# Kernel tuning notes

Hardware: AMD Instinct MI355X
Metric: run time of the kernel (lower is better)

Reference implementation:

```python
import jax, jax.numpy as jnp
import numpy as np

SEQ_LEN = 2048
EMB_DIM = 1024
HIDDEN = 1024
VOCAB = 50257
OUT = 50257


def setup_inputs() -> dict:
    key = jax.random.key(0)
    ks = jax.random.split(key, 8)
    s = 0.02
    input_seq = jax.random.randint(ks[0], (SEQ_LEN,), 0, VOCAB)
    emb = jax.random.normal(ks[1], (VOCAB, EMB_DIM), dtype=jnp.float32) * s
    # PyTorch nn.LSTM params: weight_ih [4H, E], weight_hh [4H, H], biases [4H]
    W_ih = jax.random.normal(ks[2], (4 * HIDDEN, EMB_DIM), dtype=jnp.float32) * s
    W_hh = jax.random.normal(ks[3], (4 * HIDDEN, HIDDEN), dtype=jnp.float32) * s
    b_ih = jax.random.normal(ks[4], (4 * HIDDEN,), dtype=jnp.float32) * s
    b_hh = jax.random.normal(ks[5], (4 * HIDDEN,), dtype=jnp.float32) * s
    W_out = jax.random.normal(ks[6], (OUT, HIDDEN), dtype=jnp.float32) * s
    b_out = jax.random.normal(ks[7], (OUT,), dtype=jnp.float32) * s
    return {"input_seq": input_seq, "emb": emb, "W_ih": W_ih, "W_hh": W_hh,
            "b_ih": b_ih, "b_hh": b_hh, "W_out": W_out, "b_out": b_out}


def _lstm_forward(x, W_ih, W_hh, b_ih, b_hh):
    # x: [S, E]; batch dim (=1 in the torch module) is collapsed away.
    H = W_hh.shape[1]
    # Precompute input contribution to all gates for every timestep: [S, 4H]
    x_gates = x @ W_ih.T + (b_ih + b_hh)

    def step(carry, xg):
        h, c = carry
        g = xg + h @ W_hh.T  # [4H]
        i, f, gg, o = jnp.split(g, 4)  # PyTorch gate order: i, f, g, o
        i = jax.nn.sigmoid(i)
        f = jax.nn.sigmoid(f)
        gg = jnp.tanh(gg)
        o = jax.nn.sigmoid(o)
        c = f * c + i * gg
        h = o * jnp.tanh(c)
        return (h, c), h

    h0 = jnp.zeros((H,), dtype=x.dtype)
    c0 = jnp.zeros((H,), dtype=x.dtype)
    _, hs = jax.lax.scan(step, (h0, c0), x_gates)
    return hs  # [S, H]


def reference(input_seq, emb, W_ih, W_hh, b_ih, b_hh, W_out, b_out):
    x = emb[input_seq]  # [S, E] embedding lookup
    hs = _lstm_forward(x, W_ih, W_hh, b_ih, b_hh)  # [S, H]
    logits = hs @ W_out.T + b_out  # [S, OUT]
    return jax.nn.log_softmax(logits, axis=1)
```

## Files before the change

### kernel.cpp

```cpp
#include <hip/hip_runtime.h>
#include <hip/hip_bf16.h>

#define SEQ 2048
#define EMB 1024
#define HID 1024
#define G4  4096
#define VOC 50257
#define VPAD 50304
#define KDIM 1024

typedef short bhalf8 __attribute__((ext_vector_type(8)));
typedef float f32x4  __attribute__((ext_vector_type(4)));

typedef __attribute__((address_space(3))) void lds_void;
typedef __attribute__((address_space(1))) const void gbl_cvoid;

__device__ __forceinline__ void direct_lds16(void* lds, const void* g) {
    __builtin_amdgcn_global_load_lds((gbl_cvoid*)g, (lds_void*)lds, 16, 0, 0);
}

__device__ __forceinline__ unsigned short f2b(float f) {
    unsigned u = __float_as_uint(f);
    unsigned r = u + 0x7fffu + ((u >> 16) & 1u);
    return (unsigned short)(r >> 16);
}

__global__ void f32_to_bf16_k(const float* __restrict__ src, unsigned short* __restrict__ dst,
                              long n_src, long n_dst) {
    long i = ((long)blockIdx.x * 256 + threadIdx.x) * 4;
    if (i >= n_dst) return;
    unsigned short o0 = 0, o1 = 0, o2 = 0, o3 = 0;
    if (i < n_src) {
        f32x4 v = *(const f32x4*)&src[i];
        o0 = f2b(v[0]); o1 = f2b(v[1]); o2 = f2b(v[2]); o3 = f2b(v[3]);
    }
    ushort4 o; o.x = o0; o.y = o1; o.z = o2; o.w = o3;
    *(ushort4*)&dst[i] = o;
}

__global__ void embed_cvt_k(const int* __restrict__ seq, const float* __restrict__ emb,
                            unsigned short* __restrict__ xb) {
    int s = blockIdx.x;
    int k = threadIdx.x * 4;
    long row = (long)seq[s] * EMB;
    f32x4 v = *(const f32x4*)&emb[row + k];
    ushort4 o; o.x = f2b(v[0]); o.y = f2b(v[1]); o.z = f2b(v[2]); o.w = f2b(v[3]);
    *(ushort4*)&xb[(long)s * EMB + k] = o;
}

__global__ void bias_sum_k(const float* __restrict__ a, const float* __restrict__ b,
                           float* __restrict__ o) {
    int i = blockIdx.x * 256 + threadIdx.x;
    if (i < G4) o[i] = a[i] + b[i];
}

__global__ __launch_bounds__(256)
void gemm_bt_k(const unsigned short* __restrict__ A, const unsigned short* __restrict__ Bt,
               const float* __restrict__ bias, float* __restrict__ C,
               int M, int Nreal, int K, int ldc) {
    __shared__ unsigned short lA[128 * 64];
    __shared__ unsigned short lB[128 * 64];
    const int tid  = threadIdx.x;
    const int wave = tid >> 6;
    const int lane = tid & 63;
    const int m0 = blockIdx.x * 128;
    const int n0 = blockIdx.y * 128;
    const int wm = (wave >> 1) * 64;
    const int wn = (wave & 1) * 64;
    const int quad = lane >> 4, l16 = lane & 15;
    const int srow = lane >> 3;
    const int scol = (lane & 7) * 8;

    f32x4 acc[4][4] = {};

    for (int k0 = 0; k0 < K; k0 += 64) {
#pragma unroll
        for (int c = 0; c < 4; ++c) {
            int r0 = wave * 32 + c * 8;
            const unsigned short* ga = A  + (long)(m0 + r0 + srow) * K + k0 + scol;
            direct_lds16(&lA[r0 * 64], ga);
            const unsigned short* gb = Bt + (long)(n0 + r0 + srow) * K + k0 + scol;
            direct_lds16(&lB[r0 * 64], gb);
        }
        __syncthreads();
#pragma unroll
        for (int kk = 0; kk < 2; ++kk) {
            bhalf8 af[4], bf[4];
#pragma unroll
            for (int i = 0; i < 4; ++i) {
                af[i] = *(const bhalf8*)&lA[(wm + i * 16 + l16) * 64 + kk * 32 + quad * 8];
                bf[i] = *(const bhalf8*)&lB[(wn + i * 16 + l16) * 64 + kk * 32 + quad * 8];
            }
#pragma unroll
            for (int i = 0; i < 4; ++i)
#pragma unroll
                for (int j = 0; j < 4; ++j)
                    acc[i][j] = __builtin_amdgcn_mfma_f32_16x16x32_bf16(af[i], bf[j], acc[i][j], 0, 0, 0);
        }
        __syncthreads();
    }
#pragma unroll
    for (int i = 0; i < 4; ++i) {
        int gm = m0 + wm + i * 16 + quad * 4;
#pragma unroll
        for (int j = 0; j < 4; ++j) {
            int gn = n0 + wn + j * 16 + l16;
            if (gn < Nreal) {
                float bv = bias[gn];
#pragma unroll
                for (int r = 0; r < 4; ++r)
                    C[(long)(gm + r) * ldc + gn] = acc[i][j][r] + bv;
            }
        }
    }
}

__global__ __launch_bounds__(256, 1)
void lstm_seq_k(const float* __restrict__ W_hh, const float* __restrict__ xg,
                unsigned short* __restrict__ hs_b, unsigned long long* __restrict__ hbuf) {
    const int tid = threadIdx.x;
    const int wg  = blockIdx.x;
    const int lr  = tid >> 4;
    const int seg = tid & 15;
    const int gate = lr >> 2;
    const int ul   = lr & 3;
    const int u    = wg * 4 + ul;
    const int grow = gate * HID + u;

    __shared__ float h_lds[HID];
    __shared__ float g_lds[4][4];

    f32x4 w[16];
#pragma unroll
    for (int m = 0; m < 16; ++m)
        w[m] = *(const f32x4*)&W_hh[(long)grow * HID + (m * 16 + seg) * 4];

#pragma unroll
    for (int q = 0; q < 4; ++q) h_lds[tid + q * 256] = 0.f;
    float c = 0.f;
    __syncthreads();

    for (int t = 0; t < SEQ; ++t) {
        float xgv = (seg == 0) ? xg[(long)t * G4 + grow] : 0.f;
        if (t > 0) {
            const unsigned long long want = (unsigned long long)t;
            unsigned long long* src = &hbuf[((t - 1) & 1) * HID];
#pragma unroll
            for (int q = 0; q < 4; ++q) {
                int e = tid + q * 256;
                unsigned long long v;
                do {
                    v = __hip_atomic_load(&src[e], __ATOMIC_RELAXED, __HIP_MEMORY_SCOPE_AGENT);
                } while ((v >> 32) != want);
                h_lds[e] = __uint_as_float((unsigned)v);
            }
        }
        __syncthreads();

        float acc = 0.f;
        const f32x4* h4 = (const f32x4*)h_lds;
#pragma unroll
        for (int m = 0; m < 16; ++m) {
            f32x4 hv = h4[m * 16 + seg];
            acc += w[m][0] * hv[0] + w[m][1] * hv[1] + w[m][2] * hv[2] + w[m][3] * hv[3];
        }
        acc += __shfl_xor(acc, 8);
        acc += __shfl_xor(acc, 4);
        acc += __shfl_xor(acc, 2);
        acc += __shfl_xor(acc, 1);

        if (seg == 0) {
            float g = acc + xgv;
            float a = (gate == 2) ? tanhf(g) : 1.f / (1.f + __expf(-g));
            g_lds[gate][ul] = a;
        }
        __syncthreads();
        if (tid < 4) {
            float iv = g_lds[0][tid], fv = g_lds[1][tid], gv = g_lds[2][tid], ov = g_lds[3][tid];
            c = fv * c + iv * gv;
            float h = ov * tanhf(c);
            int ug = wg * 4 + tid;
            hs_b[(long)t * HID + ug] = f2b(h);
            unsigned long long pk = ((unsigned long long)(t + 1) << 32) | (unsigned long long)__float_as_uint(h);
            __hip_atomic_store(&hbuf[(t & 1) * HID + ug], pk, __ATOMIC_RELAXED, __HIP_MEMORY_SCOPE_AGENT);
        }
        __syncthreads();
    }
}

__global__ __launch_bounds__(256)
void log_softmax_k(float* __restrict__ X) {
    const int tid = threadIdx.x;
    const long base = (long)blockIdx.x * VOC;
    float* p = X + base;
    const int head = (4 - (int)(base & 3)) & 3;
    const int n4 = (VOC - head) >> 2;
    const int tail_start = head + n4 * 4;
    f32x4* p4 = (f32x4*)(p + head);

    float m = -INFINITY, s = 0.f;
    auto upd = [&](float x) {
        float nm = fmaxf(m, x);
        s = s * __expf(m - nm) + __expf(x - nm);
        m = nm;
    };
    for (int i = tid; i < n4; i += 256) {
        f32x4 v = p4[i];
        upd(v[0]); upd(v[1]); upd(v[2]); upd(v[3]);
    }
    if (tid == 0) {
        for (int i = 0; i < head; ++i) upd(p[i]);
        for (int i = tail_start; i < VOC; ++i) upd(p[i]);
    }
#pragma unroll
    for (int o = 32; o; o >>= 1) {
        float m2 = __shfl_xor(m, o), s2 = __shfl_xor(s, o);
        float nm = fmaxf(m, m2);
        s = s * __expf(m - nm) + s2 * __expf(m2 - nm);
        m = nm;
    }
    __shared__ float sm[4], ss[4], sL;
    if ((tid & 63) == 0) { sm[tid >> 6] = m; ss[tid >> 6] = s; }
    __syncthreads();
    if (tid == 0) {
        m = sm[0]; s = ss[0];
        for (int wv = 1; wv < 4; ++wv) {
            float m2 = sm[wv], s2 = ss[wv];
            float nm = fmaxf(m, m2);
            s = s * __expf(m - nm) + s2 * __expf(m2 - nm);
            m = nm;
        }
        sL = m + __logf(s);
    }
    __syncthreads();
    const float L = sL;
    for (int i = tid; i < n4; i += 256) {
        f32x4 v = p4[i];
        v[0] -= L; v[1] -= L; v[2] -= L; v[3] -= L;
        p4[i] = v;
    }
    if (tid == 0) {
        for (int i = 0; i < head; ++i) p[i] -= L;
        for (int i = tail_start; i < VOC; ++i) p[i] -= L;
    }
}

extern "C" void kernel_launch(void* const* d_in, const int* in_sizes, int n_in,
                              void* d_out, int out_size, void* d_ws, size_t ws_size,
                              hipStream_t stream) {
    const int*   seq   = (const int*)d_in[0];
    const float* emb   = (const float*)d_in[1];
    const float* W_ih  = (const float*)d_in[2];
    const float* W_hh  = (const float*)d_in[3];
    const float* b_ih  = (const float*)d_in[4];
    const float* b_hh  = (const float*)d_in[5];
    const float* W_out = (const float*)d_in[6];
    const float* b_out = (const float*)d_in[7];
    float* out = (float*)d_out;

    size_t off = 0;
    auto carve = [&](size_t bytes) {
        void* p = (char*)d_ws + off;
        off += (bytes + 255) & ~(size_t)255;
        return p;
    };
    unsigned short* wWout = (unsigned short*)carve((size_t)VPAD * KDIM * 2);
    unsigned short* wWih  = (unsigned short*)carve((size_t)G4 * KDIM * 2);
    unsigned short* wX    = (unsigned short*)carve((size_t)SEQ * EMB * 2);
    unsigned short* wHs   = (unsigned short*)carve((size_t)SEQ * HID * 2);
    float*          wXg   = (float*)carve((size_t)SEQ * G4 * 4);
    float*          wBsum = (float*)carve((size_t)G4 * 4);
    unsigned long long* wHbuf = (unsigned long long*)carve((size_t)2 * HID * 8);

    f32_to_bf16_k<<<(int)(((size_t)VPAD * KDIM / 4 + 255) / 256), 256, 0, stream>>>(
        W_out, wWout, (long)VOC * KDIM, (long)VPAD * KDIM);
    f32_to_bf16_k<<<(int)(((size_t)G4 * KDIM / 4 + 255) / 256), 256, 0, stream>>>(
        W_ih, wWih, (long)G4 * KDIM, (long)G4 * KDIM);
    embed_cvt_k<<<SEQ, 256, 0, stream>>>(seq, emb, wX);
    bias_sum_k<<<(G4 + 255) / 256, 256, 0, stream>>>(b_ih, b_hh, wBsum);

    gemm_bt_k<<<dim3(SEQ / 128, G4 / 128), 256, 0, stream>>>(
        wX, wWih, wBsum, wXg, SEQ, G4, KDIM, G4);

    lstm_seq_k<<<256, 256, 0, stream>>>(W_hh, wXg, wHs, wHbuf);

    gemm_bt_k<<<dim3(SEQ / 128, VPAD / 128), 256, 0, stream>>>(
        wHs, wWout, b_out, out, SEQ, VOC, KDIM, VOC);

    log_softmax_k<<<SEQ, 256, 0, stream>>>(out);
}
```

Before: 6.388 ms.

## Restructure LSTM step so each wave owns one unit, cutting barriers per step

```diff
diff --git a/kernel.cpp b/kernel.cpp
--- a/kernel.cpp
+++ b/kernel.cpp
@@ -23,6 +23,13 @@
     unsigned u = __float_as_uint(f);
     unsigned r = u + 0x7fffu + ((u >> 16) & 1u);
     return (unsigned short)(r >> 16);
+}
+
+__device__ __forceinline__ float fast_sig(float x) {
+    return __frcp_rn(1.f + __expf(-x));
+}
+__device__ __forceinline__ float fast_tanh(float x) {
+    return 1.f - 2.f * __frcp_rn(__expf(2.f * x) + 1.f);
 }
 
 __global__ void f32_to_bf16_k(const float* __restrict__ src, unsigned short* __restrict__ dst,
@@ -118,73 +125,92 @@
 __global__ __launch_bounds__(256, 1)
 void lstm_seq_k(const float* __restrict__ W_hh, const float* __restrict__ xg,
                 unsigned short* __restrict__ hs_b, unsigned long long* __restrict__ hbuf) {
-    const int tid = threadIdx.x;
-    const int wg  = blockIdx.x;
-    const int lr  = tid >> 4;
-    const int seg = tid & 15;
-    const int gate = lr >> 2;
-    const int ul   = lr & 3;
-    const int u    = wg * 4 + ul;
-    const int grow = gate * HID + u;
-
-    __shared__ float h_lds[HID];
-    __shared__ float g_lds[4][4];
-
-    f32x4 w[16];
-#pragma unroll
-    for (int m = 0; m < 16; ++m)
-        w[m] = *(const f32x4*)&W_hh[(long)grow * HID + (m * 16 + seg) * 4];
-
-#pragma unroll
-    for (int q = 0; q < 4; ++q) h_lds[tid + q * 256] = 0.f;
+    const int tid  = threadIdx.x;
+    const int wg   = blockIdx.x;
+    const int wave = tid >> 6;
+    const int lane = tid & 63;
+    const int u    = wg * 4 + wave;
+
+    __shared__ float h_lds[2][HID];
+
+    f32x4 w[4][4];
+#pragma unroll
+    for (int g = 0; g < 4; ++g)
+#pragma unroll
+        for (int m = 0; m < 4; ++m)
+            w[g][m] = *(const f32x4*)&W_hh[(long)(g * HID + u) * HID + (m * 64 + lane) * 4];
+
+#pragma unroll
+    for (int q = 0; q < 4; ++q) h_lds[0][tid + q * 256] = 0.f;
     float c = 0.f;
+
+    float xc0 = xg[0 * HID + u];
+    float xc1 = xg[1 * HID + u];
+    float xc2 = xg[2 * HID + u];
+    float xc3 = xg[3 * HID + u];
     __syncthreads();
 
     for (int t = 0; t < SEQ; ++t) {
-        float xgv = (seg == 0) ? xg[(long)t * G4 + grow] : 0.f;
+        const int pb = t & 1;
         if (t > 0) {
             const unsigned long long want = (unsigned long long)t;
-            unsigned long long* src = &hbuf[((t - 1) & 1) * HID];
-#pragma unroll
-            for (int q = 0; q < 4; ++q) {
-                int e = tid + q * 256;
-                unsigned long long v;
-                do {
-                    v = __hip_atomic_load(&src[e], __ATOMIC_RELAXED, __HIP_MEMORY_SCOPE_AGENT);
-                } while ((v >> 32) != want);
-                h_lds[e] = __uint_as_float((unsigned)v);
+            unsigned long long* src = &hbuf[(pb ^ 1) * HID];
+            unsigned long long v0, v1, v2, v3;
+            for (;;) {
+                v0 = __hip_atomic_load(&src[tid],       __ATOMIC_RELAXED, __HIP_MEMORY_SCOPE_AGENT);
+                v1 = __hip_atomic_load(&src[tid + 256], __ATOMIC_RELAXED, __HIP_MEMORY_SCOPE_AGENT);
+                v2 = __hip_atomic_load(&src[tid + 512], __ATOMIC_RELAXED, __HIP_MEMORY_SCOPE_AGENT);
+                v3 = __hip_atomic_load(&src[tid + 768], __ATOMIC_RELAXED, __HIP_MEMORY_SCOPE_AGENT);
+                if (((v0 >> 32) == want) & ((v1 >> 32) == want) &
+                    ((v2 >> 32) == want) & ((v3 >> 32) == want)) break;
             }
+            float* hb = h_lds[pb];
+            hb[tid]       = __uint_as_float((unsigned)v0);
+            hb[tid + 256] = __uint_as_float((unsigned)v1);
+            hb[tid + 512] = __uint_as_float((unsigned)v2);
+            hb[tid + 768] = __uint_as_float((unsigned)v3);
         }
         __syncthreads();
 
-        float acc = 0.f;
-        const f32x4* h4 = (const f32x4*)h_lds;
-#pragma unroll
-        for (int m = 0; m < 16; ++m) {
-            f32x4 hv = h4[m * 16 + seg];
-            acc += w[m][0] * hv[0] + w[m][1] * hv[1] + w[m][2] * hv[2] + w[m][3] * hv[3];
-        }
-        acc += __shfl_xor(acc, 8);
-        acc += __shfl_xor(acc, 4);
-        acc += __shfl_xor(acc, 2);
-        acc += __shfl_xor(acc, 1);
-
-        if (seg == 0) {
-            float g = acc + xgv;
-            float a = (gate == 2) ? tanhf(g) : 1.f / (1.f + __expf(-g));
-            g_lds[gate][ul] = a;
-        }
-        __syncthreads();
-        if (tid < 4) {
-            float iv = g_lds[0][tid], fv = g_lds[1][tid], gv = g_lds[2][tid], ov = g_lds[3][tid];
-            c = fv * c + iv * gv;
-            float h = ov * tanhf(c);
-            int ug = wg * 4 + tid;
-            hs_b[(long)t * HID + ug] = f2b(h);
-            unsigned long long pk = ((unsigned long long)(t + 1) << 32) | (unsigned long long)__float_as_uint(h);
-            __hip_atomic_store(&hbuf[(t & 1) * HID + ug], pk, __ATOMIC_RELAXED, __HIP_MEMORY_SCOPE_AGENT);
-        }
-        __syncthreads();
+        float xn0 = 0.f, xn1 = 0.f, xn2 = 0.f, xn3 = 0.f;
+        if (t + 1 < SEQ) {
+            const float* xr = xg + (long)(t + 1) * G4;
+            xn0 = xr[0 * HID + u]; xn1 = xr[1 * HID + u];
+            xn2 = xr[2 * HID + u]; xn3 = xr[3 * HID + u];
+        }
+
+        const f32x4* h4 = (const f32x4*)h_lds[pb];
+        float acc0 = 0.f, acc1 = 0.f, acc2 = 0.f, acc3 = 0.f;
+#pragma unroll
+        for (int m = 0; m < 4; ++m) {
+            f32x4 hv = h4[m * 64 + lane];
+            acc0 += w[0][m][0] * hv[0] + w[0][m][1] * hv[1] + w[0][m][2] * hv[2] + w[0][m][3] * hv[3];
+            acc1 += w[1][m][0] * hv[0] + w[1][m][1] * hv[1] + w[1][m][2] * hv[2] + w[1][m][3] * hv[3];
+            acc2 += w[2][m][0] * hv[0] + w[2][m][1] * hv[1] + w[2][m][2] * hv[2] + w[2][m][3] * hv[3];
+            acc3 += w[3][m][0] * hv[0] + w[3][m][1] * hv[1] + w[3][m][2] * hv[2] + w[3][m][3] * hv[3];
+        }
+#pragma unroll
+        for (int o = 1; o < 64; o <<= 1) {
+            acc0 += __shfl_xor(acc0, o);
+            acc1 += __shfl_xor(acc1, o);
+            acc2 += __shfl_xor(acc2, o);
+            acc3 += __shfl_xor(acc3, o);
+        }
+
+        float iv = fast_sig(acc0 + xc0);
+        float fv = fast_sig(acc1 + xc1);
+        float gv = fast_tanh(acc2 + xc2);
+        float ov = fast_sig(acc3 + xc3);
+        c = fv * c + iv * gv;
+        float h = ov * fast_tanh(c);
+
+        if (lane == 0) {
+            hs_b[(long)t * HID + u] = f2b(h);
+            unsigned long long pk = ((unsigned long long)(t + 1) << 32) |
+                                    (unsigned long long)__float_as_uint(h);
+            __hip_atomic_store(&hbuf[pb * HID + u], pk, __ATOMIC_RELAXED, __HIP_MEMORY_SCOPE_AGENT);
+        }
+        xc0 = xn0; xc1 = xn1; xc2 = xn2; xc3 = xn3;
     }
 }
 
```

After: 9.627 ms. +50.7%, slower.
